# Kernel tuning notes

Hardware: AMD Instinct MI355X
Metric: run time of the kernel (lower is better)

## Reference

```python
import jax, jax.numpy as jnp
import numpy as np

N, E, F, L, G, C = 100000, 1600000, 128, 3, 512, 40
BN_EPS = 1e-5


def gcn_conv(x, src, dst, W, b, n_nodes):
    # PyG GCNConv: linear transform, symmetric normalization with self-loops,
    # scatter-add aggregation, then bias.
    xw = x @ W                                   # [N, H]
    deg = jnp.zeros((n_nodes,), x.dtype).at[dst].add(1.0) + 1.0  # +1 self-loop
    dinv = jax.lax.rsqrt(deg)                    # D^{-1/2}
    norm = dinv[src] * dinv[dst]                 # [E]
    msg = xw[src] * norm[:, None]                # gather + scale, [E, H]
    agg = jnp.zeros_like(xw).at[dst].add(msg)    # scatter-add to destinations
    agg = agg + xw * (dinv * dinv)[:, None]      # self-loop contribution
    return agg + b


def setup_inputs() -> dict:
    key = jax.random.key(0)
    ks = jax.random.split(key, 6)
    x = jax.random.normal(ks[0], (N, F), dtype=jnp.float32)
    edge_index = jax.random.randint(ks[1], (2, E), 0, N, dtype=jnp.int64)
    batch = jnp.sort(jax.random.randint(ks[2], (N,), 0, G, dtype=jnp.int64))
    conv_w = jax.random.normal(ks[3], (L, F, F), dtype=jnp.float32) * 0.05
    conv_b = jnp.zeros((L, F), dtype=jnp.float32)
    bn_gamma = jnp.ones((L, F), dtype=jnp.float32)
    bn_beta = jnp.zeros((L, F), dtype=jnp.float32)
    bn_mean = jnp.zeros((L, F), dtype=jnp.float32)
    bn_var = jnp.ones((L, F), dtype=jnp.float32)
    lin_w = jax.random.normal(ks[4], (F, C), dtype=jnp.float32) * 0.05
    lin_b = jnp.zeros((C,), dtype=jnp.float32)
    return {"x": x, "edge_index": edge_index, "batch": batch,
            "conv_w": conv_w, "conv_b": conv_b,
            "bn_gamma": bn_gamma, "bn_beta": bn_beta,
            "bn_mean": bn_mean, "bn_var": bn_var,
            "lin_w": lin_w, "lin_b": lin_b}


def reference(x, edge_index, batch, conv_w, conv_b, bn_gamma, bn_beta,
              bn_mean, bn_var, lin_w, lin_b):
    src, dst = edge_index[0], edge_index[1]
    h = x
    # layers 0..L-2: conv -> BN(eval) -> ReLU (dropout is identity in eval)
    for i in range(L - 1):
        h = gcn_conv(h, src, dst, conv_w[i], conv_b[i], N)
        h = (h - bn_mean[i]) * (bn_gamma[i] * jax.lax.rsqrt(bn_var[i] + BN_EPS)) + bn_beta[i]
        h = jax.nn.relu(h)
    # last conv (no BN/ReLU)
    h = gcn_conv(h, src, dst, conv_w[L - 1], conv_b[L - 1], N)
    # global_mean_pool over graphs
    sums = jnp.zeros((G, F), h.dtype).at[batch].add(h)
    counts = jnp.zeros((G,), h.dtype).at[batch].add(1.0)
    pooled = sums / jnp.maximum(counts, 1.0)[:, None]   # [G, F]
    return pooled @ lin_w + lin_b                        # [G, C]
```

## Files before the change

kernel.cpp:

```cpp
#include <hip/hip_runtime.h>

#define Nn 100000
#define Ee 1600000
#define Ff 128
#define Gg 512
#define Cc 40
#define NB 1563
#define PAD 32

__global__ void prep_scales_k(const float* __restrict__ conv_b,
                              const float* __restrict__ gamma,
                              const float* __restrict__ beta,
                              const float* __restrict__ mean,
                              const float* __restrict__ var,
                              float* __restrict__ sc, float* __restrict__ sh)
{
    int i = blockIdx.x * blockDim.x + threadIdx.x;
    if (i >= 3 * Ff) return;
    float b = conv_b[i];
    if (i < 2 * Ff) {
        float s = gamma[i] * rsqrtf(var[i] + 1e-5f);
        sc[i] = s;
        sh[i] = (b - mean[i]) * s + beta[i];
    } else {
        sc[i] = 1.0f;
        sh[i] = b;
    }
}

__global__ void bucket_count_k(const int* __restrict__ dst, int* __restrict__ bcnt)
{
    int e = blockIdx.x * 256 + threadIdx.x;
    if (e < Ee) atomicAdd(&bcnt[(dst[e] >> 6) * PAD], 1);
}

__global__ void scan_buckets_k(const int* __restrict__ bcnt, int* __restrict__ bktOff,
                               int* __restrict__ off)
{
    __shared__ int tot[256];
    int t = threadIdx.x;
    int v[7]; int s = 0;
    #pragma unroll
    for (int j = 0; j < 7; ++j) {
        int idx = t * 7 + j;
        int val = (idx < NB) ? bcnt[idx * PAD] : 0;
        v[j] = val; s += val;
    }
    tot[t] = s;
    __syncthreads();
    for (int d = 1; d < 256; d <<= 1) {
        int x = (t >= d) ? tot[t - d] : 0;
        __syncthreads();
        tot[t] += x;
        __syncthreads();
    }
    int base = tot[t] - s;
    #pragma unroll
    for (int j = 0; j < 7; ++j) {
        int idx = t * 7 + j;
        if (idx < NB) bktOff[idx] = base;
        base += v[j];
    }
    if (t == 255) { bktOff[NB] = base; off[Nn] = base; }
}

__global__ void bucket_fill_k(const int* __restrict__ src, const int* __restrict__ dst,
                              const int* __restrict__ bktOff, int* __restrict__ bcur,
                              int* __restrict__ staged)
{
    int e = blockIdx.x * 256 + threadIdx.x;
    if (e < Ee) {
        int d = dst[e];
        int b = d >> 6;
        int p = atomicAdd(&bcur[b * PAD], 1);
        staged[bktOff[b] + p] = src[e] | ((d & 63) << 17);
    }
}

__global__ __launch_bounds__(256) void bucket_scatter_k(
    const int* __restrict__ staged, const int* __restrict__ bktOff,
    int* __restrict__ off, float* __restrict__ dinv, int* __restrict__ csrc)
{
    __shared__ int cl[64], ol[64], cu[64];
    const int b = blockIdx.x, tid = threadIdx.x;
    const int base = bktOff[b], base2 = bktOff[b + 1];
    if (tid < 64) cl[tid] = 0;
    __syncthreads();
    for (int i = base + tid; i < base2; i += 256)
        atomicAdd(&cl[staged[i] >> 17], 1);
    __syncthreads();
    if (tid == 0) {
        int r = 0;
        #pragma unroll
        for (int l = 0; l < 64; ++l) { ol[l] = r; r += cl[l]; }
    }
    __syncthreads();
    if (tid < 64) {
        int node = b * 64 + tid;
        if (node < Nn) {
            off[node]  = base + ol[tid];
            dinv[node] = rsqrtf((float)cl[tid] + 1.0f);
        }
        cu[tid] = 0;
    }
    __syncthreads();
    for (int i = base + tid; i < base2; i += 256) {
        int w = staged[i];
        int l = w >> 17;
        int pos = atomicAdd(&cu[l], 1);
        csrc[base + ol[l] + pos] = w & 0x1FFFF;
    }
}

__global__ __launch_bounds__(256) void gemm_scale_k(
    const float* __restrict__ A, const float* __restrict__ W,
    const float* __restrict__ dinv, float* __restrict__ Y, int n)
{
    const int tid  = threadIdx.x;
    const int half = __builtin_amdgcn_readfirstlane(tid >> 7);
    const int cb   = half * 64;
    const int r    = blockIdx.x * 128 + (tid & 127);
    const int rr   = min(r, n - 1);
    const float4* Ap = (const float4*)(A + ((size_t)rr << 7));
    const float*  Wp = W + cb;

    float acc[64];
    #pragma unroll
    for (int c = 0; c < 64; ++c) acc[c] = 0.f;

    for (int kc = 0; kc < 4; ++kc) {
        float4 a[8];
        #pragma unroll
        for (int i = 0; i < 8; ++i) a[i] = Ap[kc * 8 + i];
        const float* af = reinterpret_cast<const float*>(a);
        #pragma unroll
        for (int kk = 0; kk < 32; ++kk) {
            const float av = af[kk];
            const float* wr = Wp + (kc * 32 + kk) * Ff;
            #pragma unroll
            for (int c = 0; c < 64; ++c)
                acc[c] = fmaf(av, wr[c], acc[c]);
        }
    }

    if (r < n) {
        const float di = dinv[r];
        float* yp = Y + ((size_t)r << 7) + cb;
        #pragma unroll
        for (int c = 0; c < 64; c += 4)
            *(float4*)(yp + c) = make_float4(acc[c] * di, acc[c + 1] * di,
                                             acc[c + 2] * di, acc[c + 3] * di);
    }
}

__global__ __launch_bounds__(256) void aggregate_k(
    const float* __restrict__ Y, const int* __restrict__ off,
    const int* __restrict__ srcs, const float* __restrict__ dinv,
    const float* __restrict__ sc, const float* __restrict__ sh,
    float* __restrict__ H, int dorelu, int n)
{
    int wid  = threadIdx.x >> 6;
    int lane = threadIdx.x & 63;
    int node = blockIdx.x * 4 + wid;
    if (node >= n) return;
    int beg = off[node], end = off[node + 1];
    int c = lane * 2;

    float2 self = *(const float2*)(Y + (size_t)node * Ff + c);
    float ax = self.x, ay = self.y;
    float bx = 0.f,    by = 0.f;

    for (int e = beg; e < end; e += 64) {
        int nb = min(64, end - e);
        int sidx = (lane < nb) ? srcs[e + lane] : 0;
        int j = 0;
        for (; j + 4 <= nb; j += 4) {
            int s0 = __shfl(sidx, j);
            int s1 = __shfl(sidx, j + 1);
            int s2 = __shfl(sidx, j + 2);
            int s3 = __shfl(sidx, j + 3);
            float2 v0 = *(const float2*)(Y + (size_t)s0 * Ff + c);
            float2 v1 = *(const float2*)(Y + (size_t)s1 * Ff + c);
            float2 v2 = *(const float2*)(Y + (size_t)s2 * Ff + c);
            float2 v3 = *(const float2*)(Y + (size_t)s3 * Ff + c);
            ax += v0.x; ay += v0.y; bx += v1.x; by += v1.y;
            ax += v2.x; ay += v2.y; bx += v3.x; by += v3.y;
        }
        for (; j < nb; ++j) {
            int s0 = __shfl(sidx, j);
            float2 v0 = *(const float2*)(Y + (size_t)s0 * Ff + c);
            ax += v0.x; ay += v0.y;
        }
    }
    float di = dinv[node];
    float2 scv = *(const float2*)(sc + c);
    float2 shv = *(const float2*)(sh + c);
    float ox = (ax + bx) * di * scv.x + shv.x;
    float oy = (ay + by) * di * scv.y + shv.y;
    if (dorelu) { ox = fmaxf(ox, 0.f); oy = fmaxf(oy, 0.f); }
    *(float2*)(H + (size_t)node * Ff + c) = make_float2(ox, oy);
}

__global__ __launch_bounds__(128) void pool_linear_k(
    const float* __restrict__ H, const int* __restrict__ batch,
    const float* __restrict__ lw, const float* __restrict__ lb,
    float* __restrict__ out)
{
    int g = blockIdx.x, f = threadIdx.x;
    int lo = 0, hi = Nn;
    while (lo < hi) { int m = (lo + hi) >> 1; if (batch[m] < g) lo = m + 1; else hi = m; }
    int start = lo;
    hi = Nn;
    while (lo < hi) { int m = (lo + hi) >> 1; if (batch[m] < g + 1) lo = m + 1; else hi = m; }
    int end = lo;

    float a0 = 0.f, a1 = 0.f, a2 = 0.f, a3 = 0.f;
    int i = start;
    for (; i + 4 <= end; i += 4) {
        a0 += H[(size_t)(i + 0) * Ff + f];
        a1 += H[(size_t)(i + 1) * Ff + f];
        a2 += H[(size_t)(i + 2) * Ff + f];
        a3 += H[(size_t)(i + 3) * Ff + f];
    }
    for (; i < end; ++i) a0 += H[(size_t)i * Ff + f];
    int cnt = end - start;
    __shared__ float pooled[Ff];
    pooled[f] = ((a0 + a1) + (a2 + a3)) / (float)max(cnt, 1);
    __syncthreads();
    if (f < Cc) {
        float o = lb[f];
        #pragma unroll 8
        for (int k = 0; k < Ff; ++k) o += pooled[k] * lw[k * Cc + f];
        out[g * Cc + f] = o;
    }
}

extern "C" void kernel_launch(void* const* d_in, const int* in_sizes, int n_in,
                              void* d_out, int out_size, void* d_ws, size_t ws_size,
                              hipStream_t stream)
{
    const float* x      = (const float*)d_in[0];
    const int*   ei     = (const int*)d_in[1];
    const int*   batch  = (const int*)d_in[2];
    const float* conv_w = (const float*)d_in[3];
    const float* conv_b = (const float*)d_in[4];
    const float* gamma  = (const float*)d_in[5];
    const float* beta   = (const float*)d_in[6];
    const float* mean   = (const float*)d_in[7];
    const float* var    = (const float*)d_in[8];
    const float* lw     = (const float*)d_in[9];
    const float* lb     = (const float*)d_in[10];
    float* out = (float*)d_out;

    const int* srcp = ei;
    const int* dstp = ei + Ee;

    float* h      = (float*)d_ws;
    float* y      = h + (size_t)Nn * Ff;
    float* dinv   = y + (size_t)Nn * Ff;
    float* sc     = dinv + Nn;
    float* sh     = sc + 3 * Ff;
    int*   bcnt   = (int*)(sh + 3 * Ff);
    int*   bcur   = bcnt + NB * PAD;
    int*   off    = bcur + NB * PAD;
    int*   csrc   = off + (Nn + 1);
    int*   bktOff = csrc + Ee;
    int*   staged = (int*)y;

    hipMemsetAsync(bcnt, 0, (size_t)(2 * NB * PAD) * sizeof(int), stream);

    prep_scales_k<<<2, 256, 0, stream>>>(conv_b, gamma, beta, mean, var, sc, sh);
    bucket_count_k<<<Ee / 256, 256, 0, stream>>>(dstp, bcnt);
    scan_buckets_k<<<1, 256, 0, stream>>>(bcnt, bktOff, off);
    bucket_fill_k<<<Ee / 256, 256, 0, stream>>>(srcp, dstp, bktOff, bcur, staged);
    bucket_scatter_k<<<NB, 256, 0, stream>>>(staged, bktOff, off, dinv, csrc);

    const int gemm_grid = (Nn + 127) / 128;
    const int agg_grid  = (Nn + 3) / 4;
    for (int l = 0; l < 3; ++l) {
        const float* in = (l == 0) ? x : h;
        gemm_scale_k<<<gemm_grid, 256, 0, stream>>>(in, conv_w + (size_t)l * Ff * Ff,
                                                    dinv, y, Nn);
        aggregate_k<<<agg_grid, 256, 0, stream>>>(
            y, off, csrc, dinv, sc + l * Ff, sh + l * Ff,
            h, (l < 2) ? 1 : 0, Nn);
    }
    pool_linear_k<<<Gg, 128, 0, stream>>>(h, batch, lw, lb, out);
}
```

Before: 834.0 us.

## Privatize bucket counting and fill with shared-memory histograms per block

Bucket count and fill kernels now process 6250 edges per 1024-thread block, counting into a shared-memory histogram of all buckets and then issuing one global atomic per nonzero bucket per block. The fill kernel reserves a contiguous range per bucket per block, then writes staged entries at local offsets. This cuts global atomic contention from one per edge to roughly one per bucket per block. The cost is fewer blocks (256), heavier shared-memory use, and per-thread register arrays.

```diff
diff --git a/kernel.cpp b/kernel.cpp
--- a/kernel.cpp
+++ b/kernel.cpp
@@ -7,6 +7,8 @@
 #define Cc 40
 #define NB 1563
 #define PAD 32
+#define FB 256
+#define EPB 6250
 
 __global__ void prep_scales_k(const float* __restrict__ conv_b,
                               const float* __restrict__ gamma,
@@ -28,10 +30,24 @@
     }
 }
 
-__global__ void bucket_count_k(const int* __restrict__ dst, int* __restrict__ bcnt)
-{
-    int e = blockIdx.x * 256 + threadIdx.x;
-    if (e < Ee) atomicAdd(&bcnt[(dst[e] >> 6) * PAD], 1);
+__global__ __launch_bounds__(1024) void bucket_count_k(
+    const int* __restrict__ dst, int* __restrict__ bcnt)
+{
+    __shared__ int cnt[NB];
+    const int t = threadIdx.x;
+    for (int b = t; b < NB; b += 1024) cnt[b] = 0;
+    __syncthreads();
+    const int e0 = blockIdx.x * EPB;
+    #pragma unroll
+    for (int j = 0; j < 7; ++j) {
+        int e = e0 + t + j * 1024;
+        if (e < e0 + EPB) atomicAdd(&cnt[dst[e] >> 6], 1);
+    }
+    __syncthreads();
+    for (int b = t; b < NB; b += 1024) {
+        int c = cnt[b];
+        if (c) atomicAdd(&bcnt[b * PAD], c);
+    }
 }
 
 __global__ void scan_buckets_k(const int* __restrict__ bcnt, int* __restrict__ bktOff,
@@ -64,16 +80,40 @@
     if (t == 255) { bktOff[NB] = base; off[Nn] = base; }
 }
 
-__global__ void bucket_fill_k(const int* __restrict__ src, const int* __restrict__ dst,
-                              const int* __restrict__ bktOff, int* __restrict__ bcur,
-                              int* __restrict__ staged)
-{
-    int e = blockIdx.x * 256 + threadIdx.x;
-    if (e < Ee) {
-        int d = dst[e];
-        int b = d >> 6;
-        int p = atomicAdd(&bcur[b * PAD], 1);
-        staged[bktOff[b] + p] = src[e] | ((d & 63) << 17);
+__global__ __launch_bounds__(1024) void bucket_fill_k(
+    const int* __restrict__ src, const int* __restrict__ dst,
+    const int* __restrict__ bktOff, int* __restrict__ bcur,
+    int* __restrict__ staged)
+{
+    __shared__ int cnt[NB];
+    __shared__ int gb[NB];
+    const int t = threadIdx.x;
+    for (int b = t; b < NB; b += 1024) cnt[b] = 0;
+    __syncthreads();
+    const int e0 = blockIdx.x * EPB;
+    int bb[7], lp[7], pl[7];
+    #pragma unroll
+    for (int j = 0; j < 7; ++j) {
+        int e = e0 + t + j * 1024;
+        bb[j] = -1;
+        if (e < e0 + EPB) {
+            int d = dst[e];
+            int b = d >> 6;
+            bb[j] = b;
+            lp[j] = atomicAdd(&cnt[b], 1);
+            pl[j] = src[e] | ((d & 63) << 17);
+        }
+    }
+    __syncthreads();
+    for (int b = t; b < NB; b += 1024) {
+        int c = cnt[b];
+        gb[b] = c ? atomicAdd(&bcur[b * PAD], c) : 0;
+    }
+    __syncthreads();
+    #pragma unroll
+    for (int j = 0; j < 7; ++j) {
+        int b = bb[j];
+        if (b >= 0) staged[bktOff[b] + gb[b] + lp[j]] = pl[j];
     }
 }
 
@@ -270,9 +310,9 @@
     hipMemsetAsync(bcnt, 0, (size_t)(2 * NB * PAD) * sizeof(int), stream);
 
     prep_scales_k<<<2, 256, 0, stream>>>(conv_b, gamma, beta, mean, var, sc, sh);
-    bucket_count_k<<<Ee / 256, 256, 0, stream>>>(dstp, bcnt);
+    bucket_count_k<<<FB, 1024, 0, stream>>>(dstp, bcnt);
     scan_buckets_k<<<1, 256, 0, stream>>>(bcnt, bktOff, off);
-    bucket_fill_k<<<Ee / 256, 256, 0, stream>>>(srcp, dstp, bktOff, bcur, staged);
+    bucket_fill_k<<<FB, 1024, 0, stream>>>(srcp, dstp, bktOff, bcur, staged);
     bucket_scatter_k<<<NB, 256, 0, stream>>>(staged, bktOff, off, dinv, csrc);
 
     const int gemm_grid = (Nn + 127) / 128;
```

Result: faster. 733.2 us (-12.1%).
